# Kernel tuning notes

Hardware: AMD Instinct MI355X
Metric: run time of the kernel (lower is better)

## Reference

```python
import jax, jax.numpy as jnp
import numpy as np

STRIDES = (2, 2, 2, 2)
ALPHA = 1.0
NEG_SLOPE = 0.1


def _conv1d(h, w, b, stride):
    # h: (N, C, L), w: (O, I, K) -> (N, O, L_out), VALID padding
    out = jax.lax.conv_general_dilated(
        h, w, window_strides=(stride,), padding='VALID',
        dimension_numbers=('NCH', 'OIH', 'NCH'))
    return out + b[None, :, None]


def setup_inputs() -> dict:
    key = jax.random.key(0)
    ks = jax.random.split(key, 10)
    N, C, L = 256, 128, 1024
    k_sizes = (15, 12, 7, 4)
    inp = {'x': jax.random.normal(ks[0], (N, C, L), dtype=jnp.float32)}
    for i, k in enumerate(k_sizes):
        fan_in = C * k
        scale = 1.0 / np.sqrt(fan_in).astype(np.float32)
        inp[f'w{i+1}'] = jax.random.normal(ks[1 + 2 * i], (C, C, k), dtype=jnp.float32) * scale
        inp[f'b{i+1}'] = jax.random.normal(ks[2 + 2 * i], (C,), dtype=jnp.float32) * 0.01
    D = C * 59  # flattened encoder output: 1024->505->247->121->59
    inp['centers'] = jax.random.normal(ks[9], (64, D), dtype=jnp.float32)
    return inp


def reference(x, w1, b1, w2, b2, w3, b3, w4, b4, centers):
    ws = [(w1, b1), (w2, b2), (w3, b3), (w4, b4)]
    h = x
    for i, ((w, b), s) in enumerate(zip(ws, STRIDES)):
        h = _conv1d(h, w, b, s)
        if i != len(ws) - 1:
            h = jnp.where(h > 0, h, NEG_SLOPE * h)  # LeakyReLU(0.1)
    z = h.reshape(h.shape[0], -1)  # (N, D)
    # squared distances via norm expansion: ||z||^2 + ||c||^2 - 2 z.c
    d2 = (jnp.sum(z * z, axis=1, keepdims=True)
          + jnp.sum(centers * centers, axis=1)[None, :]
          - 2.0 * z @ centers.T)  # (N, K)
    q = 1.0 / (1.0 + d2 / ALPHA)
    q = q ** ((ALPHA + 1.0) / 2.0)
    q = q / jnp.sum(q, axis=1, keepdims=True)
    return q
```

## Files before the change

kernel.cpp:

```cpp
#include <hip/hip_runtime.h>

typedef __bf16 bf16;
typedef __bf16 bf16x4 __attribute__((ext_vector_type(4)));
typedef __bf16 bf16x8 __attribute__((ext_vector_type(8)));
typedef float f32x4 __attribute__((ext_vector_type(4)));

#define CCH 128

__global__ void k_prep_all(const float* __restrict__ w1, const float* __restrict__ w2,
                           const float* __restrict__ w3, const float* __restrict__ w4,
                           const float* __restrict__ cen,
                           bf16* __restrict__ o1, bf16* __restrict__ o2,
                           bf16* __restrict__ o3, bf16* __restrict__ o4,
                           bf16* __restrict__ cpk, float* __restrict__ cc) {
    __shared__ float red[256];
    int tid = threadIdx.x;
    int bid = blockIdx.x;
    if (bid < 2432) {
        int idx = bid * 256 + tid;
        const float* src; bf16* dst; int Kw; int r = idx;
        if (r < 15 * 16384) { src = w1; dst = o1; Kw = 15; }
        else if ((r -= 15 * 16384) < 12 * 16384) { src = w2; dst = o2; Kw = 12; }
        else if ((r -= 12 * 16384) < 7 * 16384) { src = w3; dst = o3; Kw = 7; }
        else if ((r -= 7 * 16384) < 4 * 16384) { src = w4; dst = o4; Kw = 4; }
        else return;
        int e = r & 7, lane = (r >> 3) & 63, og = (r >> 9) & 7, c = (r >> 12) & 3, kt = r >> 14;
        int o = og * 16 + (lane & 15);
        int i = c * 32 + (lane >> 4) * 8 + e;
        dst[r] = (bf16)src[(o * 128 + i) * Kw + kt];
    } else if (bid < 2432 + 256) {
        int j = bid - 2432;
        int l = j >> 2;
#pragma unroll
        for (int it = 0; it < 8; ++it) {
            int u = tid + it * 256;
            int og = u >> 9, r9 = u & 511;
            int lane = r9 >> 3, e = r9 & 7;
            int k = og * 16 + (lane & 15);
            int oc = (j & 3) * 32 + (lane >> 4) * 8 + e;
            float v = (l < 59) ? cen[k * 7552 + oc * 59 + l] : 0.f;
            cpk[(((size_t)(j * 4 + og)) << 9) + r9] = (bf16)v;
        }
    } else {
        int k = bid - (2432 + 256);
        float s = 0.f;
        for (int idx = tid; idx < 8192; idx += 256) {
            int l = idx >> 7;
            int o = idx & 127;
            if (l < 59) {
                float fv = (float)(bf16)cen[k * 7552 + o * 59 + l];
                s += fv * fv;
            }
        }
        red[tid] = s;
        __syncthreads();
        for (int st = 128; st > 0; st >>= 1) {
            if (tid < st) red[tid] += red[tid + st];
            __syncthreads();
        }
        if (tid == 0) cc[k] = red[0];
    }
}

__global__ __launch_bounds__(256, 4) void k_conv1(
    const float* __restrict__ x, const bf16* __restrict__ wTp,
    const float* __restrict__ bias, bf16* __restrict__ out) {
    constexpr int KW = 15, LT = 128, PH = 2, OUT_ROWS = 512;
    constexpr int P = (LT - 1) * 2 + KW;
    constexpr int KC = 2;
    constexpr int RS = 64;
    constexpr int NLT = LT / 16;
    constexpr int ESE = 136;
    constexpr int SMELE = (P * RS > LT * ESE) ? P * RS : LT * ESE;
    constexpr int NJ = KW * KC;
    __shared__ __align__(16) bf16 smem[SMELE];

    const int n = blockIdx.y;
    const int l0 = blockIdx.x * LT;
    const int p0 = l0 * 2;
    const int tid = threadIdx.x;
    const int wid = tid >> 6;
    const int lane = tid & 63;
    const int quad = lane >> 4;
    const int l15 = lane & 15;
    const int og0 = wid * 2;

    f32x4 acc[2][NLT];
#pragma unroll
    for (int a = 0; a < 2; ++a)
#pragma unroll
        for (int b = 0; b < NLT; ++b) acc[a][b] = (f32x4){0.f, 0.f, 0.f, 0.f};

    bf16x8 afr[2][2];
    const bf16* wbase = wTp + (size_t)lane * 8;
    afr[0][0] = *(const bf16x8*)(wbase + ((size_t)(og0 + 0) << 9));
    afr[0][1] = *(const bf16x8*)(wbase + ((size_t)(og0 + 1) << 9));

    const int cst = tid >> 2;
    const int qw = tid & 3;

#pragma unroll 1
    for (int ph = 0; ph < PH; ++ph) {
        if (ph) __syncthreads();

        const float* bch = x + ((size_t)(n * 128 + ph * 64 + cst)) * 1024;
#pragma unroll 4
        for (int it = 0; it < 17; ++it) {
            int pp = it * 16 + qw * 4;
            int gp = p0 + pp;
            f32x4 t;
            if (gp + 3 < 1024) {
                t = *(const f32x4*)(bch + gp);
            } else {
#pragma unroll
                for (int e = 0; e < 4; ++e) t[e] = (gp + e < 1024) ? bch[gp + e] : 0.f;
            }
#pragma unroll
            for (int e = 0; e < 4; ++e) {
                int ppe = pp + e;
                int sc8 = (((cst >> 3) ^ ((ppe >> 1) & 7)) << 3) | (cst & 7);
                smem[ppe * RS + sc8] = (bf16)t[e];
            }
        }
        __syncthreads();

#pragma unroll 2
        for (int j = 0; j < NJ; ++j) {
            int nj = j + 1, nph = ph;
            if (nj == NJ) { nj = 0; ++nph; }
            if (nph < PH) {
                int kt1 = nj >> 1;
                int c1 = (nj & (KC - 1)) + nph * KC;
                const bf16* wp = wbase + ((size_t)((kt1 * 4 + c1) * 8 + og0) << 9);
                afr[(j + 1) & 1][0] = *(const bf16x8*)(wp);
                afr[(j + 1) & 1][1] = *(const bf16x8*)(wp + 512);
            }
            const int kt = j >> 1;
            const int c16l = (j & (KC - 1)) * 4 + quad;
#pragma unroll
            for (int lt = 0; lt < NLT; ++lt) {
                int p = (lt * 16 + l15) * 2 + kt;
                int sc = c16l ^ ((p >> 1) & 7);
                bf16x8 bfr = *(const bf16x8*)(smem + p * RS + sc * 8);
                acc[0][lt] = __builtin_amdgcn_mfma_f32_16x16x32_bf16(
                    afr[j & 1][0], bfr, acc[0][lt], 0, 0, 0);
                acc[1][lt] = __builtin_amdgcn_mfma_f32_16x16x32_bf16(
                    afr[j & 1][1], bfr, acc[1][lt], 0, 0, 0);
            }
        }
    }

    __syncthreads();
#pragma unroll
    for (int ot = 0; ot < 2; ++ot) {
        const int o0 = wid * 32 + ot * 16 + quad * 4;
        const f32x4 bv = *(const f32x4*)(bias + o0);
#pragma unroll
        for (int lt = 0; lt < NLT; ++lt) {
            const int l = lt * 16 + l15;
            bf16x4 pk;
#pragma unroll
            for (int r = 0; r < 4; ++r) {
                float v = acc[ot][lt][r] + bv[r];
                v = (v > 0.f) ? v : 0.1f * v;
                pk[r] = (bf16)v;
            }
            *(bf16x4*)(smem + l * ESE + o0) = pk;
        }
    }
    __syncthreads();
    constexpr int SNIT = LT * 16 / 256;
    bf16* op = out + ((size_t)n * OUT_ROWS + l0) * CCH;
#pragma unroll
    for (int it = 0; it < SNIT; ++it) {
        int u = tid + it * 256;
        int l = u >> 4;
        int g = u & 15;
        *(bf16x8*)(op + l * CCH + g * 8) = *(const bf16x8*)(smem + l * ESE + g * 8);
    }
}

__global__ __launch_bounds__(512, 1) void k_fused234(
    const bf16* __restrict__ h1g, const bf16* __restrict__ wT2,
    const bf16* __restrict__ wT3, const bf16* __restrict__ wT4,
    const float* __restrict__ b2, const float* __restrict__ b3,
    const float* __restrict__ b4, const bf16* __restrict__ cpk,
    const float* __restrict__ cc, float* __restrict__ out) {
    __shared__ __align__(16) bf16 lds[34048 + 33536];
    __shared__ float d2p[2][64];
    __shared__ float zred[8];
    bf16* sbuf = lds;
    bf16* h2   = lds + 34048;
    bf16* h3   = lds;
    bf16* zmem = lds + 16640;

    const int n = blockIdx.x;
    const int tid = threadIdx.x;
    const int wid = tid >> 6;
    const int lane = tid & 63;
    const int quad = lane >> 4;
    const int l15 = lane & 15;

    if (tid < 96) *(f32x4*)(h2 + 256 * 128 + tid * 8) = (f32x4){0.f, 0.f, 0.f, 0.f};

    {
        const int w4 = wid & 3;
        const int g = wid >> 2;
        const int og0 = w4 * 2;
        const bf16* w2base = wT2 + (size_t)lane * 8;
        const bf16* base = h1g + (size_t)n * 512 * 128;
        constexpr int NJ2 = 48;

        auto conv2_compute = [&](int s) {
            f32x4 acc[2][4];
#pragma unroll
            for (int a = 0; a < 2; ++a)
#pragma unroll
                for (int b = 0; b < 4; ++b) acc[a][b] = (f32x4){0.f, 0.f, 0.f, 0.f};
            bf16x8 afr[2][2];
            afr[0][0] = *(const bf16x8*)(w2base + ((size_t)og0 << 9));
            afr[0][1] = *(const bf16x8*)(w2base + ((size_t)(og0 + 1) << 9));
#pragma unroll 2
            for (int j = 0; j < NJ2; ++j) {
                if (j + 1 < NJ2) {
                    int kt1 = (j + 1) >> 2, c1 = (j + 1) & 3;
                    const bf16* wp = w2base + ((size_t)((kt1 * 4 + c1) * 8 + og0) << 9);
                    afr[(j + 1) & 1][0] = *(const bf16x8*)(wp);
                    afr[(j + 1) & 1][1] = *(const bf16x8*)(wp + 512);
                }
                int kt = j >> 2;
                int c16l = (j & 3) * 4 + quad;
#pragma unroll
                for (int lt = 0; lt < 4; ++lt) {
                    int p = (g * 64 + lt * 16 + l15) * 2 + kt;
                    int sc = (c16l & 8) | ((c16l & 7) ^ ((p >> 1) & 7));
                    bf16x8 bfr = *(const bf16x8*)(sbuf + p * 128 + sc * 8);
                    acc[0][lt] = __builtin_amdgcn_mfma_f32_16x16x32_bf16(
                        afr[j & 1][0], bfr, acc[0][lt], 0, 0, 0);
                    acc[1][lt] = __builtin_amdgcn_mfma_f32_16x16x32_bf16(
                        afr[j & 1][1], bfr, acc[1][lt], 0, 0, 0);
                }
            }
#pragma unroll
            for (int ot = 0; ot < 2; ++ot) {
                int o0 = (og0 + ot) * 16 + quad * 4;
                f32x4 bv = *(const f32x4*)(b2 + o0);
                int c = o0 >> 3;
#pragma unroll
                for (int lt = 0; lt < 4; ++lt) {
                    int l = s * 128 + g * 64 + lt * 16 + l15;
                    bf16x4 pk;
#pragma unroll
                    for (int r = 0; r < 4; ++r) {
                        float v = acc[ot][lt][r] + bv[r];
                        v = (v > 0.f) ? v : 0.1f * v;
                        pk[r] = (bf16)v;
                    }
                    int sc = (c & 8) | ((c & 7) ^ ((l >> 1) & 7));
                    *(bf16x4*)(h2 + l * 128 + sc * 8 + (o0 & 7)) = pk;
                }
            }
        };

#pragma unroll
        for (int it = 0; it < 9; ++it) {
            int u = tid + it * 512;
            if (u < 266 * 16) {
                int p = u >> 4, c = u & 15;
                bf16x8 t = *(const bf16x8*)(base + (size_t)p * 128 + c * 8);
                int sc = (c & 8) | ((c & 7) ^ ((p >> 1) & 7));
                *(bf16x8*)(sbuf + p * 128 + sc * 8) = t;
            }
        }
        bf16x8 nb[9];
#pragma unroll
        for (int it = 0; it < 9; ++it) {
            int u = tid + it * 512;
            if (u < 266 * 16) {
                int p = u >> 4, c = u & 15;
                int prow = 256 + p; if (prow > 511) prow = 511;
                nb[it] = *(const bf16x8*)(base + (size_t)prow * 128 + c * 8);
            }
        }
        __syncthreads();

        conv2_compute(0);
        __syncthreads();
#pragma unroll
        for (int it = 0; it < 9; ++it) {
            int u = tid + it * 512;
            if (u < 266 * 16) {
                int p = u >> 4, c = u & 15;
                int sc = (c & 8) | ((c & 7) ^ ((p >> 1) & 7));
                *(bf16x8*)(sbuf + p * 128 + sc * 8) = nb[it];
            }
        }
        __syncthreads();
        conv2_compute(1);
        __syncthreads();
    }

    {
        if (tid < 32) *(f32x4*)(h3 + 128 * 128 + tid * 8) = (f32x4){0.f, 0.f, 0.f, 0.f};
        const int og0 = (wid & 3) * 2;
        const int ph3 = wid >> 2;
        const bf16* w3base = wT3 + (size_t)lane * 8;
        constexpr int NJ3 = 28;
        f32x4 acc[2][4];
#pragma unroll
        for (int a = 0; a < 2; ++a)
#pragma unroll
            for (int b = 0; b < 4; ++b) acc[a][b] = (f32x4){0.f, 0.f, 0.f, 0.f};
        bf16x8 afr[2][2];
        afr[0][0] = *(const bf16x8*)(w3base + ((size_t)og0 << 9));
        afr[0][1] = *(const bf16x8*)(w3base + ((size_t)(og0 + 1) << 9));
#pragma unroll 2
        for (int j = 0; j < NJ3; ++j) {
            if (j + 1 < NJ3) {
                int kt1 = (j + 1) >> 2, c1 = (j + 1) & 3;
                const bf16* wp = w3base + ((size_t)((kt1 * 4 + c1) * 8 + og0) << 9);
                afr[(j + 1) & 1][0] = *(const bf16x8*)(wp);
                afr[(j + 1) & 1][1] = *(const bf16x8*)(wp + 512);
            }
            int kt = j >> 2;
            int c16l = (j & 3) * 4 + quad;
#pragma unroll
            for (int lt = 0; lt < 4; ++lt) {
                int p = (ph3 * 64 + lt * 16 + l15) * 2 + kt;
                int sc = (c16l & 8) | ((c16l & 7) ^ ((p >> 1) & 7));
                bf16x8 bfr = *(const bf16x8*)(h2 + p * 128 + sc * 8);
                acc[0][lt] = __builtin_amdgcn_mfma_f32_16x16x32_bf16(
                    afr[j & 1][0], bfr, acc[0][lt], 0, 0, 0);
                acc[1][lt] = __builtin_amdgcn_mfma_f32_16x16x32_bf16(
                    afr[j & 1][1], bfr, acc[1][lt], 0, 0, 0);
            }
        }
        __syncthreads();
#pragma unroll
        for (int ot = 0; ot < 2; ++ot) {
            int o0 = (og0 + ot) * 16 + quad * 4;
            f32x4 bv = *(const f32x4*)(b3 + o0);
            int c = o0 >> 3;
#pragma unroll
            for (int lt = 0; lt < 4; ++lt) {
                int l = ph3 * 64 + lt * 16 + l15;
                bf16x4 pk;
#pragma unroll
                for (int r = 0; r < 4; ++r) {
                    float v = acc[ot][lt][r] + bv[r];
                    v = (v > 0.f) ? v : 0.1f * v;
                    pk[r] = (bf16)v;
                }
                int sc = (c & 8) | ((c & 7) ^ ((l >> 1) & 7));
                *(bf16x4*)(h3 + l * 128 + sc * 8 + (o0 & 7)) = pk;
            }
        }
    }
    __syncthreads();

    {
        f32x4 acc[4];
#pragma unroll
        for (int b = 0; b < 4; ++b) acc[b] = (f32x4){0.f, 0.f, 0.f, 0.f};
        bf16x8 afr[2];
        const bf16* w4base = wT4 + (size_t)lane * 8;
        afr[0] = *(const bf16x8*)(w4base + ((size_t)wid << 9));
        constexpr int NJ4 = 16;
#pragma unroll 2
        for (int j = 0; j < NJ4; ++j) {
            if (j + 1 < NJ4) {
                int kt1 = (j + 1) >> 2, c1 = (j + 1) & 3;
                afr[(j + 1) & 1] =
                    *(const bf16x8*)(w4base + ((size_t)((kt1 * 4 + c1) * 8 + wid) << 9));
            }
            int kt = j >> 2;
            int c16l = (j & 3) * 4 + quad;
#pragma unroll
            for (int lt = 0; lt < 4; ++lt) {
                int p = (lt * 16 + l15) * 2 + kt;
                int sc = (c16l & 8) | ((c16l & 7) ^ ((p >> 1) & 7));
                bf16x8 bfr = *(const bf16x8*)(h3 + p * 128 + sc * 8);
                acc[lt] = __builtin_amdgcn_mfma_f32_16x16x32_bf16(afr[j & 1], bfr, acc[lt], 0, 0, 0);
            }
        }
        const int o0 = wid * 16 + quad * 4;
        const f32x4 bv = *(const f32x4*)(b4 + o0);
        float s2 = 0.f;
#pragma unroll
        for (int lt = 0; lt < 4; ++lt) {
            const int l = lt * 16 + l15;
            bf16x4 pk;
#pragma unroll
            for (int r = 0; r < 4; ++r) {
                float v = acc[lt][r] + bv[r];
                pk[r] = (l < 59) ? (bf16)v : (bf16)0.f;
                float zf = (float)pk[r];
                s2 += zf * zf;
            }
            *(bf16x4*)(zmem + l * 136 + o0) = pk;
        }
#pragma unroll
        for (int o = 32; o > 0; o >>= 1) s2 += __shfl_xor(s2, o);
        if (lane == 0) zred[wid] = s2;
    }
    __syncthreads();

    {
        const int og = wid & 3;
        const int h = wid >> 2;
        const bf16* cb = cpk + ((size_t)og << 9) + (size_t)lane * 8;
        f32x4 acc = (f32x4){0.f, 0.f, 0.f, 0.f};
        const int j0 = h * 128;
        bf16x8 af[4];
#pragma unroll
        for (int q = 0; q < 4; ++q)
            af[q] = *(const bf16x8*)(cb + ((size_t)(j0 + q) << 11));
#pragma unroll 4
        for (int jj = 0; jj < 128; ++jj) {
            bf16x8 a = af[jj & 3];
            if (jj + 4 < 128)
                af[jj & 3] = *(const bf16x8*)(cb + ((size_t)(j0 + jj + 4) << 11));
            int l = h * 32 + (jj >> 2);
            int off = (jj & 3) * 32 + quad * 8;
            bf16x8 b = *(const bf16x8*)(zmem + l * 136 + off);
            acc = __builtin_amdgcn_mfma_f32_16x16x32_bf16(a, b, acc, 0, 0, 0);
        }
        if (l15 == 0) {
#pragma unroll
            for (int r = 0; r < 4; ++r) d2p[h][og * 16 + quad * 4 + r] = acc[r];
        }
    }
    __syncthreads();

    if (tid < 64) {
        float zc = d2p[0][tid] + d2p[1][tid];
        float z2 = zred[0] + zred[1] + zred[2] + zred[3]
                 + zred[4] + zred[5] + zred[6] + zred[7];
        float d2v = z2 + cc[tid] - 2.f * zc;
        float q = 1.f / (1.f + d2v);
        float tot = q;
#pragma unroll
        for (int o = 32; o > 0; o >>= 1) tot += __shfl_xor(tot, o);
        out[n * 64 + tid] = q / tot;
    }
}

extern "C" void kernel_launch(void* const* d_in, const int* in_sizes, int n_in,
                              void* d_out, int out_size, void* d_ws, size_t ws_size,
                              hipStream_t stream) {
    (void)in_sizes; (void)n_in; (void)out_size; (void)ws_size;
    const float* x   = (const float*)d_in[0];
    const float* w1  = (const float*)d_in[1];
    const float* b1  = (const float*)d_in[2];
    const float* w2  = (const float*)d_in[3];
    const float* b2  = (const float*)d_in[4];
    const float* w3  = (const float*)d_in[5];
    const float* b3  = (const float*)d_in[6];
    const float* w4  = (const float*)d_in[7];
    const float* b4  = (const float*)d_in[8];
    const float* cen = (const float*)d_in[9];
    float* out = (float*)d_out;

    char* ws = (char*)d_ws;
    size_t off = 0;
    auto alloc = [&](size_t bytes) -> void* {
        void* p = ws + off;
        off += (bytes + 255) & ~(size_t)255;
        return p;
    };
    bf16* wT1 = (bf16*)alloc((size_t)15 * 16384 * sizeof(bf16));
    bf16* wT2 = (bf16*)alloc((size_t)12 * 16384 * sizeof(bf16));
    bf16* wT3 = (bf16*)alloc((size_t)7 * 16384 * sizeof(bf16));
    bf16* wT4 = (bf16*)alloc((size_t)4 * 16384 * sizeof(bf16));
    bf16* cpk = (bf16*)alloc((size_t)1024 * 512 * sizeof(bf16));
    float* cc = (float*)alloc(64 * sizeof(float));
    bf16* h1  = (bf16*)alloc((size_t)256 * 512 * 128 * sizeof(bf16));
    (void)alloc((size_t)1 << 20);

    k_prep_all<<<2432 + 256 + 64, 256, 0, stream>>>(w1, w2, w3, w4, cen,
                                                    wT1, wT2, wT3, wT4, cpk, cc);
    k_conv1<<<dim3(4, 256), 256, 0, stream>>>(x, wT1, b1, h1);
    k_fused234<<<256, 512, 0, stream>>>(h1, wT2, wT3, wT4, b2, b3, b4, cpk, cc, out);
}
```

Measured before the change: 324.3 us.

## Retile conv2-4 warps to 4 output tiles by 2 position tiles, reload input in loop

Each warp now covers four output-channel tiles and fewer position tiles (wid split into output half and row group) in conv2, conv3 and conv4. The aim is to cut LDS reads of activation fragments per MFMA, while each warp loads more weight fragments from global. The conv2 second-half prefetch into registers is replaced by a plain loop that reloads sbuf each half. That lowers register pressure but drops the overlap of the global load with compute.

```diff
diff --git a/kernel.cpp b/kernel.cpp
--- a/kernel.cpp
+++ b/kernel.cpp
@@ -200,59 +200,74 @@
     const int lane = tid & 63;
     const int quad = lane >> 4;
     const int l15 = lane & 15;
+    const int oh = wid & 1;
+    const int rg = wid >> 1;
 
     if (tid < 96) *(f32x4*)(h2 + 256 * 128 + tid * 8) = (f32x4){0.f, 0.f, 0.f, 0.f};
 
     {
-        const int w4 = wid & 3;
-        const int g = wid >> 2;
-        const int og0 = w4 * 2;
-        const bf16* w2base = wT2 + (size_t)lane * 8;
+        const bf16* w2base = wT2 + (size_t)lane * 8 + ((size_t)(oh * 4) << 9);
         const bf16* base = h1g + (size_t)n * 512 * 128;
         constexpr int NJ2 = 48;
-
-        auto conv2_compute = [&](int s) {
-            f32x4 acc[2][4];
-#pragma unroll
-            for (int a = 0; a < 2; ++a)
-#pragma unroll
-                for (int b = 0; b < 4; ++b) acc[a][b] = (f32x4){0.f, 0.f, 0.f, 0.f};
-            bf16x8 afr[2][2];
-            afr[0][0] = *(const bf16x8*)(w2base + ((size_t)og0 << 9));
-            afr[0][1] = *(const bf16x8*)(w2base + ((size_t)(og0 + 1) << 9));
+#pragma unroll 1
+        for (int s = 0; s < 2; ++s) {
+            if (s) __syncthreads();
+#pragma unroll
+            for (int it = 0; it < 9; ++it) {
+                int u = tid + it * 512;
+                if (u < 266 * 16) {
+                    int p = u >> 4, c = u & 15;
+                    int prow = s * 256 + p; if (prow > 511) prow = 511;
+                    bf16x8 t = *(const bf16x8*)(base + (size_t)prow * 128 + c * 8);
+                    int sc = (c & 8) | ((c & 7) ^ ((p >> 1) & 7));
+                    *(bf16x8*)(sbuf + p * 128 + sc * 8) = t;
+                }
+            }
+            __syncthreads();
+
+            f32x4 acc[4][2];
+#pragma unroll
+            for (int a = 0; a < 4; ++a)
+#pragma unroll
+                for (int b = 0; b < 2; ++b) acc[a][b] = (f32x4){0.f, 0.f, 0.f, 0.f};
+            bf16x8 afr[2][4];
+#pragma unroll
+            for (int a = 0; a < 4; ++a)
+                afr[0][a] = *(const bf16x8*)(w2base + ((size_t)a << 9));
 #pragma unroll 2
             for (int j = 0; j < NJ2; ++j) {
                 if (j + 1 < NJ2) {
                     int kt1 = (j + 1) >> 2, c1 = (j + 1) & 3;
-                    const bf16* wp = w2base + ((size_t)((kt1 * 4 + c1) * 8 + og0) << 9);
-                    afr[(j + 1) & 1][0] = *(const bf16x8*)(wp);
-                    afr[(j + 1) & 1][1] = *(const bf16x8*)(wp + 512);
+                    const bf16* wp = w2base + ((size_t)((kt1 * 4 + c1) * 8) << 9);
+#pragma unroll
+                    for (int a = 0; a < 4; ++a)
+                        afr[(j + 1) & 1][a] = *(const bf16x8*)(wp + ((size_t)a << 9));
                 }
                 int kt = j >> 2;
                 int c16l = (j & 3) * 4 + quad;
 #pragma unroll
-                for (int lt = 0; lt < 4; ++lt) {
-                    int p = (g * 64 + lt * 16 + l15) * 2 + kt;
+                for (int lt = 0; lt < 2; ++lt) {
+                    int p = (rg * 32 + lt * 16 + l15) * 2 + kt;
                     int sc = (c16l & 8) | ((c16l & 7) ^ ((p >> 1) & 7));
                     bf16x8 bfr = *(const bf16x8*)(sbuf + p * 128 + sc * 8);
-                    acc[0][lt] = __builtin_amdgcn_mfma_f32_16x16x32_bf16(
-                        afr[j & 1][0], bfr, acc[0][lt], 0, 0, 0);
-                    acc[1][lt] = __builtin_amdgcn_mfma_f32_16x16x32_bf16(
-                        afr[j & 1][1], bfr, acc[1][lt], 0, 0, 0);
+#pragma unroll
+                    for (int a = 0; a < 4; ++a)
+                        acc[a][lt] = __builtin_amdgcn_mfma_f32_16x16x32_bf16(
+                            afr[j & 1][a], bfr, acc[a][lt], 0, 0, 0);
                 }
             }
 #pragma unroll
-            for (int ot = 0; ot < 2; ++ot) {
-                int o0 = (og0 + ot) * 16 + quad * 4;
+            for (int a = 0; a < 4; ++a) {
+                int o0 = (oh * 4 + a) * 16 + quad * 4;
                 f32x4 bv = *(const f32x4*)(b2 + o0);
                 int c = o0 >> 3;
 #pragma unroll
-                for (int lt = 0; lt < 4; ++lt) {
-                    int l = s * 128 + g * 64 + lt * 16 + l15;
+                for (int lt = 0; lt < 2; ++lt) {
+                    int l = s * 128 + rg * 32 + lt * 16 + l15;
                     bf16x4 pk;
 #pragma unroll
                     for (int r = 0; r < 4; ++r) {
-                        float v = acc[ot][lt][r] + bv[r];
+                        float v = acc[a][lt][r] + bv[r];
                         v = (v > 0.f) ? v : 0.1f * v;
                         pk[r] = (bf16)v;
                     }
@@ -260,94 +275,58 @@
                     *(bf16x4*)(h2 + l * 128 + sc * 8 + (o0 & 7)) = pk;
                 }
             }
-        };
-
-#pragma unroll
-        for (int it = 0; it < 9; ++it) {
-            int u = tid + it * 512;
-            if (u < 266 * 16) {
-                int p = u >> 4, c = u & 15;
-                bf16x8 t = *(const bf16x8*)(base + (size_t)p * 128 + c * 8);
-                int sc = (c & 8) | ((c & 7) ^ ((p >> 1) & 7));
-                *(bf16x8*)(sbuf + p * 128 + sc * 8) = t;
-            }
-        }
-        bf16x8 nb[9];
-#pragma unroll
-        for (int it = 0; it < 9; ++it) {
-            int u = tid + it * 512;
-            if (u < 266 * 16) {
-                int p = u >> 4, c = u & 15;
-                int prow = 256 + p; if (prow > 511) prow = 511;
-                nb[it] = *(const bf16x8*)(base + (size_t)prow * 128 + c * 8);
-            }
-        }
-        __syncthreads();
-
-        conv2_compute(0);
-        __syncthreads();
-#pragma unroll
-        for (int it = 0; it < 9; ++it) {
-            int u = tid + it * 512;
-            if (u < 266 * 16) {
-                int p = u >> 4, c = u & 15;
-                int sc = (c & 8) | ((c & 7) ^ ((p >> 1) & 7));
-                *(bf16x8*)(sbuf + p * 128 + sc * 8) = nb[it];
-            }
-        }
-        __syncthreads();
-        conv2_compute(1);
+        }
         __syncthreads();
     }
 
     {
         if (tid < 32) *(f32x4*)(h3 + 128 * 128 + tid * 8) = (f32x4){0.f, 0.f, 0.f, 0.f};
-        const int og0 = (wid & 3) * 2;
-        const int ph3 = wid >> 2;
-        const bf16* w3base = wT3 + (size_t)lane * 8;
+        const bf16* w3base = wT3 + (size_t)lane * 8 + ((size_t)(oh * 4) << 9);
         constexpr int NJ3 = 28;
-        f32x4 acc[2][4];
-#pragma unroll
-        for (int a = 0; a < 2; ++a)
-#pragma unroll
-            for (int b = 0; b < 4; ++b) acc[a][b] = (f32x4){0.f, 0.f, 0.f, 0.f};
-        bf16x8 afr[2][2];
-        afr[0][0] = *(const bf16x8*)(w3base + ((size_t)og0 << 9));
-        afr[0][1] = *(const bf16x8*)(w3base + ((size_t)(og0 + 1) << 9));
+        f32x4 acc[4][2];
+#pragma unroll
+        for (int a = 0; a < 4; ++a)
+#pragma unroll
+            for (int b = 0; b < 2; ++b) acc[a][b] = (f32x4){0.f, 0.f, 0.f, 0.f};
+        bf16x8 afr[2][4];
+#pragma unroll
+        for (int a = 0; a < 4; ++a)
+            afr[0][a] = *(const bf16x8*)(w3base + ((size_t)a << 9));
 #pragma unroll 2
         for (int j = 0; j < NJ3; ++j) {
             if (j + 1 < NJ3) {
                 int kt1 = (j + 1) >> 2, c1 = (j + 1) & 3;
-                const bf16* wp = w3base + ((size_t)((kt1 * 4 + c1) * 8 + og0) << 9);
-                afr[(j + 1) & 1][0] = *(const bf16x8*)(wp);
-                afr[(j + 1) & 1][1] = *(const bf16x8*)(wp + 512);
+                const bf16* wp = w3base + ((size_t)((kt1 * 4 + c1) * 8) << 9);
+#pragma unroll
+                for (int a = 0; a < 4; ++a)
+                    afr[(j + 1) & 1][a] = *(const bf16x8*)(wp + ((size_t)a << 9));
             }
             int kt = j >> 2;
             int c16l = (j & 3) * 4 + quad;
 #pragma unroll
-            for (int lt = 0; lt < 4; ++lt) {
-                int p = (ph3 * 64 + lt * 16 + l15) * 2 + kt;
+            for (int lt = 0; lt < 2; ++lt) {
+                int p = (rg * 32 + lt * 16 + l15) * 2 + kt;
                 int sc = (c16l & 8) | ((c16l & 7) ^ ((p >> 1) & 7));
                 bf16x8 bfr = *(const bf16x8*)(h2 + p * 128 + sc * 8);
-                acc[0][lt] = __builtin_amdgcn_mfma_f32_16x16x32_bf16(
-                    afr[j & 1][0], bfr, acc[0][lt], 0, 0, 0);
-                acc[1][lt] = __builtin_amdgcn_mfma_f32_16x16x32_bf16(
-                    afr[j & 1][1], bfr, acc[1][lt], 0, 0, 0);
+#pragma unroll
+                for (int a = 0; a < 4; ++a)
+                    acc[a][lt] = __builtin_amdgcn_mfma_f32_16x16x32_bf16(
+                        afr[j & 1][a], bfr, acc[a][lt], 0, 0, 0);
             }
         }
         __syncthreads();
 #pragma unroll
-        for (int ot = 0; ot < 2; ++ot) {
-            int o0 = (og0 + ot) * 16 + quad * 4;
+        for (int a = 0; a < 4; ++a) {
+            int o0 = (oh * 4 + a) * 16 + quad * 4;
             f32x4 bv = *(const f32x4*)(b3 + o0);
             int c = o0 >> 3;
 #pragma unroll
-            for (int lt = 0; lt < 4; ++lt) {
-                int l = ph3 * 64 + lt * 16 + l15;
+            for (int lt = 0; lt < 2; ++lt) {
+                int l = rg * 32 + lt * 16 + l15;
                 bf16x4 pk;
 #pragma unroll
                 for (int r = 0; r < 4; ++r) {
-                    float v = acc[ot][lt][r] + bv[r];
+                    float v = acc[a][lt][r] + bv[r];
                     v = (v > 0.f) ? v : 0.1f * v;
                     pk[r] = (bf16)v;
                 }
@@ -361,38 +340,42 @@
     {
         f32x4 acc[4];
 #pragma unroll
-        for (int b = 0; b < 4; ++b) acc[b] = (f32x4){0.f, 0.f, 0.f, 0.f};
-        bf16x8 afr[2];
-        const bf16* w4base = wT4 + (size_t)lane * 8;
-        afr[0] = *(const bf16x8*)(w4base + ((size_t)wid << 9));
+        for (int a = 0; a < 4; ++a) acc[a] = (f32x4){0.f, 0.f, 0.f, 0.f};
+        bf16x8 afr[2][4];
+        const bf16* w4base = wT4 + (size_t)lane * 8 + ((size_t)(oh * 4) << 9);
+#pragma unroll
+        for (int a = 0; a < 4; ++a)
+            afr[0][a] = *(const bf16x8*)(w4base + ((size_t)a << 9));
         constexpr int NJ4 = 16;
 #pragma unroll 2
         for (int j = 0; j < NJ4; ++j) {
             if (j + 1 < NJ4) {
                 int kt1 = (j + 1) >> 2, c1 = (j + 1) & 3;
-                afr[(j + 1) & 1] =
-                    *(const bf16x8*)(w4base + ((size_t)((kt1 * 4 + c1) * 8 + wid) << 9));
+                const bf16* wp = w4base + ((size_t)((kt1 * 4 + c1) * 8) << 9);
+#pragma unroll
+                for (int a = 0; a < 4; ++a)
+                    afr[(j + 1) & 1][a] = *(const bf16x8*)(wp + ((size_t)a << 9));
             }
             int kt = j >> 2;
             int c16l = (j & 3) * 4 + quad;
-#pragma unroll
-            for (int lt = 0; lt < 4; ++lt) {
-                int p = (lt * 16 + l15) * 2 + kt;
-                int sc = (c16l & 8) | ((c16l & 7) ^ ((p >> 1) & 7));
-                bf16x8 bfr = *(const bf16x8*)(h3 + p * 128 + sc * 8);
-                acc[lt] = __builtin_amdgcn_mfma_f32_16x16x32_bf16(afr[j & 1], bfr, acc[lt], 0, 0, 0);
-            }
-        }
-        const int o0 = wid * 16 + quad * 4;
-        const f32x4 bv = *(const f32x4*)(b4 + o0);
+            int p = (rg * 16 + l15) * 2 + kt;
+            int sc = (c16l & 8) | ((c16l & 7) ^ ((p >> 1) & 7));
+            bf16x8 bfr = *(const bf16x8*)(h3 + p * 128 + sc * 8);
+#pragma unroll
+            for (int a = 0; a < 4; ++a)
+                acc[a] = __builtin_amdgcn_mfma_f32_16x16x32_bf16(
+                    afr[j & 1][a], bfr, acc[a], 0, 0, 0);
+        }
+        const int l = rg * 16 + l15;
         float s2 = 0.f;
 #pragma unroll
-        for (int lt = 0; lt < 4; ++lt) {
-            const int l = lt * 16 + l15;
+        for (int a = 0; a < 4; ++a) {
+            const int o0 = (oh * 4 + a) * 16 + quad * 4;
+            const f32x4 bv = *(const f32x4*)(b4 + o0);
             bf16x4 pk;
 #pragma unroll
             for (int r = 0; r < 4; ++r) {
-                float v = acc[lt][r] + bv[r];
+                float v = acc[a][r] + bv[r];
                 pk[r] = (l < 59) ? (bf16)v : (bf16)0.f;
                 float zf = (float)pk[r];
                 s2 += zf * zf;
```

After: 321.0 us. About the same (-1.0%).
